# Kernel optimization log

Hardware: AMD Instinct MI355X
Metric: run time of the kernel (lower is better)

Reference implementation:

```python
import jax, jax.numpy as jnp
import numpy as np

B, N, C, H, P, K = 32, 4096, 64, 256, 8, 2


def setup_inputs() -> dict:
    key = jax.random.key(0)
    k1, k2, k3, k4 = jax.random.split(key, 4)
    s1 = 1.0 / np.sqrt(C)
    s2 = 1.0 / np.sqrt(H)
    return {
        "u_t": jax.random.normal(k1, (B, N, C), dtype=jnp.float32),
        "W1": jax.random.normal(k2, (P, C, H), dtype=jnp.float32) * s1,
        "b1": jnp.zeros((P, H), dtype=jnp.float32),
        "W2": jax.random.normal(k3, (P, H, C), dtype=jnp.float32) * s2,
        "b2": jnp.zeros((P, C), dtype=jnp.float32),
        "Wr": jax.random.normal(k4, (C, P), dtype=jnp.float32) * s1,
        "br": jnp.zeros((P,), dtype=jnp.float32),
        "top_k": K,
    }


def reference(u_t, W1, b1, W2, b2, Wr, br, top_k):
    # u_state = u_t[..., :output_channels]; here C_in == output_channels
    u_state = u_t
    # Router: mean-pool over spatial points -> per-sample logits over primitives
    pooled = jnp.mean(u_state, axis=1)                     # (B, C)
    logits = pooled @ Wr + br                              # (B, P)
    topk_vals, topk_idx = jax.lax.top_k(logits, top_k)     # (B, K)
    w = jax.nn.softmax(topk_vals, axis=-1)                 # (B, K) combine weights
    # Sparse dispatch: gather only the selected experts' params per sample
    W1e = W1[topk_idx]                                     # (B, K, C, H)
    b1e = b1[topk_idx]                                     # (B, K, H)
    W2e = W2[topk_idx]                                     # (B, K, H, C)
    b2e = b2[topk_idx]                                     # (B, K, C)
    # Primitive operator: pointwise 2-layer GELU MLP (erf gelu, torch default)
    h1 = jax.nn.gelu(jnp.einsum('bnc,bkch->bknh', u_t, W1e) + b1e[:, :, None, :],
                     approximate=False)                    # (B, K, N, H)
    delta = jnp.einsum('bknh,bkhc->bknc', h1, W2e) + b2e[:, :, None, :]  # (B, K, N, C)
    # Weighted combine: delta_sum = sum_k w_k * delta_k
    delta_sum = jnp.einsum('bknc,bk->bnc', delta, w)       # (B, N, C)
    return u_state + delta_sum
```

## Files before the change

kernel.cpp:

```cpp
#include <hip/hip_runtime.h>
#include <hip/hip_bf16.h>
#include <math.h>

#define B_ 32
#define N_ 4096
#define C_ 64
#define H_ 256
#define P_ 8
#define NPOOL 1024

typedef short bf16x8 __attribute__((ext_vector_type(8)));
typedef float f32x4 __attribute__((ext_vector_type(4)));

union BF8 { bf16x8 v; unsigned int w[4]; };

__device__ __forceinline__ unsigned short f2bf(float f) {
    union { float f; unsigned int u; } v; v.f = f;
    unsigned int r = v.u + 0x7FFFu + ((v.u >> 16) & 1u);
    return (unsigned short)(r >> 16);
}
__device__ __forceinline__ float bf2f(unsigned short h) {
    union { float f; unsigned int u; } v; v.u = ((unsigned int)h) << 16; return v.f;
}
__device__ __forceinline__ unsigned int pk_bf16(float lo, float hi) {
    unsigned int r;
    asm("v_cvt_pk_bf16_f32 %0, %1, %2" : "=v"(r) : "v"(lo), "v"(hi));
    return r;
}
__device__ __forceinline__ float gelu_w(float x, float wk) {
    float x2 = x * x;
    float y2 = x * fmaf(0.10294322f, x2, 2.30220772f);
    float e  = __builtin_amdgcn_exp2f(y2);
    float rc = __builtin_amdgcn_rcpf(e + 1.0f);
    float wx = wk * x;
    return fmaf(-wx, rc, wx);
}

__device__ __forceinline__ int hperm(int t, int d) {
    return ((t >> 1) << 5) + ((d >> 2) << 3) + ((t & 1) << 2) + (d & 3);
}

__global__ void prep_pool(const float* __restrict__ W1, const float* __restrict__ W2,
                          const float* __restrict__ b1, const float* __restrict__ u,
                          const float* __restrict__ Wr, const float* __restrict__ br,
                          unsigned short* __restrict__ W1P, unsigned short* __restrict__ W2T,
                          unsigned short* __restrict__ b1P, float* __restrict__ pooled,
                          int* __restrict__ counter, float4* __restrict__ route) {
    int bid = blockIdx.x, tid = threadIdx.x;
    if (bid < 512) {
        int oi = bid * 256 + tid;
        int e = oi >> 14, rowP = (oi >> 6) & 255, c = oi & 63;
        int h = hperm(rowP >> 4, rowP & 15);
        W1P[oi] = f2bf(W1[(e << 14) + (c << 8) + h]);
        return;
    }
    if (bid < 1024) {
        int oi = (bid - 512) * 256 + tid;
        int e = oi >> 14, c = (oi >> 8) & 63, h = oi & 255;
        W2T[oi] = f2bf(W2[(e << 14) + (h << 6) + c]);
        return;
    }
    if (bid < 1032) {
        int oi = (bid - 1024) * 256 + tid;
        int e = oi >> 8, idx = oi & 255;
        int h = hperm(idx >> 4, idx & 15);
        b1P[oi] = f2bf(b1[(e << 8) + h]);
        return;
    }
    int pb = bid - 1032;
    int b = pb >> 5, chunk = pb & 31;
    int c = tid & 63, rg = tid >> 6;
    const float* base = u + ((size_t)b * N_ + (size_t)chunk * 128) * C_;
    float s = 0.f;
    #pragma unroll 4
    for (int i = 0; i < 32; ++i) s += base[(i * 4 + rg) * C_ + c];
    __shared__ float red[4][64];
    __shared__ int isLast;
    __shared__ float lgAll[B_][P_];
    red[rg][c] = s;
    __syncthreads();
    if (tid < 64) {
        float t4 = red[0][tid] + red[1][tid] + red[2][tid] + red[3][tid];
        atomicAdd(&pooled[b * C_ + tid], t4);
        __threadfence();
    }
    __syncthreads();
    if (tid == 0) {
        int old = atomicAdd(counter, 1);
        isLast = (old == NPOOL - 1);
    }
    __syncthreads();
    if (!isLast) return;
    __threadfence();
    {
        int rb = tid >> 3, p = tid & 7;
        const float* pb2 = pooled + rb * C_;
        float sacc = br[p];
        #pragma unroll
        for (int cc = 0; cc < C_; ++cc) {
            float pv = __hip_atomic_load(&pb2[cc], __ATOMIC_RELAXED, __HIP_MEMORY_SCOPE_AGENT);
            sacc += pv * (1.0f / N_) * Wr[cc * P_ + p];
        }
        lgAll[rb][p] = sacc;
    }
    __syncthreads();
    if (tid < B_) {
        float lg[P_];
        #pragma unroll
        for (int p = 0; p < P_; ++p) lg[p] = lgAll[tid][p];
        int i0 = 0;
        #pragma unroll
        for (int p = 1; p < P_; ++p) if (lg[p] > lg[i0]) i0 = p;
        int i1 = (i0 == 0) ? 1 : 0;
        #pragma unroll
        for (int p = 0; p < P_; ++p) if (p != i0 && lg[p] > lg[i1]) i1 = p;
        float e1 = __expf(lg[i1] - lg[i0]);
        float w0 = 1.f / (1.f + e1);
        route[tid] = make_float4(w0, e1 * w0, __int_as_float(i0), __int_as_float(i1));
    }
}

__global__ __launch_bounds__(256, 2)
void moe_main(const float* __restrict__ u, const unsigned short* __restrict__ W1P,
              const unsigned short* __restrict__ W2T, const unsigned short* __restrict__ b1P,
              const float* __restrict__ b2, const float4* __restrict__ route,
              float* __restrict__ out) {
    const int tid = threadIdx.x;
    const int wv = tid >> 6, lane = tid & 63;
    const int r = lane & 15, g = lane >> 4;
    const int b = blockIdx.x >> 4;
    const int nslab = ((blockIdx.x & 15) << 2) + wv;
    const int n0 = nslab << 6;

    float4 rd = route[b];
    const float wk2[2] = { rd.x, rd.y };
    const int eidx[2] = { __float_as_int(rd.z), __float_as_int(rd.w) };

    const float* ubase = u + ((size_t)b * N_ + n0) * C_;
    bf16x8 ub[4][2];
    #pragma unroll
    for (int rt = 0; rt < 4; ++rt) {
        const float* rp = ubase + (rt * 16 + r) * C_;
        #pragma unroll
        for (int ks = 0; ks < 2; ++ks) {
            float4 lo = *(const float4*)(rp + ks * 32 + g * 8);
            float4 hi = *(const float4*)(rp + ks * 32 + g * 8 + 4);
            BF8 t;
            t.w[0] = pk_bf16(lo.x, lo.y); t.w[1] = pk_bf16(lo.z, lo.w);
            t.w[2] = pk_bf16(hi.x, hi.y); t.w[3] = pk_bf16(hi.z, hi.w);
            ub[rt][ks] = t.v;
        }
    }

    f32x4 acc2[4][4];
    #pragma unroll
    for (int ct = 0; ct < 4; ++ct)
        #pragma unroll
        for (int rt = 0; rt < 4; ++rt)
            #pragma unroll
            for (int q = 0; q < 4; ++q) acc2[ct][rt][q] = 0.f;

    for (int ke = 0; ke < 2; ++ke) {
        const int e = eidx[ke];
        const float wk = wk2[ke];
        const unsigned short* w1p = W1P + (e << 14);
        const unsigned short* w2t = W2T + (e << 14);
        const unsigned short* b1e = b1P + (e << 8);

        #pragma unroll
        for (int tp = 0; tp < 8; ++tp) {
            bf16x8 a1[2][2];
            #pragma unroll
            for (int tt = 0; tt < 2; ++tt)
                #pragma unroll
                for (int ks = 0; ks < 2; ++ks)
                    a1[tt][ks] = *(const bf16x8*)(w1p + ((tp * 32 + tt * 16 + r) << 6) + ks * 32 + g * 8);
            f32x4 acc1[2][4];
            #pragma unroll
            for (int tt = 0; tt < 2; ++tt)
                #pragma unroll
                for (int rt = 0; rt < 4; ++rt)
                    #pragma unroll
                    for (int q = 0; q < 4; ++q) acc1[tt][rt][q] = 0.f;
            #pragma unroll
            for (int ks = 0; ks < 2; ++ks)
                #pragma unroll
                for (int tt = 0; tt < 2; ++tt)
                    #pragma unroll
                    for (int rt = 0; rt < 4; ++rt)
                        acc1[tt][rt] = __builtin_amdgcn_mfma_f32_16x16x32_bf16(
                            a1[tt][ks], ub[rt][ks], acc1[tt][rt], 0, 0, 0);

            float bv[8];
            {
                const unsigned short* bp = b1e + tp * 32 + 4 * g;
                #pragma unroll
                for (int j = 0; j < 4; ++j) { bv[j] = bf2f(bp[j]); bv[4 + j] = bf2f(bp[16 + j]); }
            }
            bf16x8 a2[4];
            #pragma unroll
            for (int rt = 0; rt < 4; ++rt) {
                float gv[8];
                #pragma unroll
                for (int j = 0; j < 4; ++j) {
                    gv[j]     = gelu_w(acc1[0][rt][j] + bv[j],     wk);
                    gv[4 + j] = gelu_w(acc1[1][rt][j] + bv[4 + j], wk);
                }
                BF8 t;
                t.w[0] = pk_bf16(gv[0], gv[1]); t.w[1] = pk_bf16(gv[2], gv[3]);
                t.w[2] = pk_bf16(gv[4], gv[5]); t.w[3] = pk_bf16(gv[6], gv[7]);
                a2[rt] = t.v;
            }

            bf16x8 b2f[4];
            #pragma unroll
            for (int ct = 0; ct < 4; ++ct)
                b2f[ct] = *(const bf16x8*)(w2t + ((ct * 16 + r) << 8) + tp * 32 + g * 8);
            #pragma unroll
            for (int ct = 0; ct < 4; ++ct)
                #pragma unroll
                for (int rt = 0; rt < 4; ++rt)
                    acc2[ct][rt] = __builtin_amdgcn_mfma_f32_16x16x32_bf16(
                        a2[rt], b2f[ct], acc2[ct][rt], 0, 0, 0);
        }
    }

    float bsum[4];
    #pragma unroll
    for (int ct = 0; ct < 4; ++ct) {
        int c = ct * 16 + r;
        bsum[ct] = wk2[0] * b2[eidx[0] * C_ + c] + wk2[1] * b2[eidx[1] * C_ + c];
    }
    float* obase = out + ((size_t)b * N_ + n0) * C_;
    #pragma unroll
    for (int rt = 0; rt < 4; ++rt)
        #pragma unroll
        for (int j = 0; j < 4; ++j) {
            int row = rt * 16 + 4 * g + j;
            #pragma unroll
            for (int ct = 0; ct < 4; ++ct) {
                int c = ct * 16 + r;
                obase[row * C_ + c] = ubase[row * C_ + c] + acc2[ct][rt][j] + bsum[ct];
            }
        }
}

extern "C" void kernel_launch(void* const* d_in, const int* in_sizes, int n_in,
                              void* d_out, int out_size, void* d_ws, size_t ws_size,
                              hipStream_t stream) {
    const float* u  = (const float*)d_in[0];
    const float* W1 = (const float*)d_in[1];
    const float* b1 = (const float*)d_in[2];
    const float* W2 = (const float*)d_in[3];
    const float* b2 = (const float*)d_in[4];
    const float* Wr = (const float*)d_in[5];
    const float* br = (const float*)d_in[6];
    float* out = (float*)d_out;

    char* ws = (char*)d_ws;
    float* pooled        = (float*)ws;
    int* counter         = (int*)(ws + 8192);
    float4* route        = (float4*)(ws + 8256);
    unsigned short* b1P  = (unsigned short*)(ws + 8768);
    unsigned short* W1P  = (unsigned short*)(ws + 16384);
    unsigned short* W2T  = (unsigned short*)(ws + 16384 + 262144);

    hipMemsetAsync(ws, 0, 8256, stream);
    prep_pool<<<2056, 256, 0, stream>>>(W1, W2, b1, u, Wr, br, W1P, W2T, b1P, pooled, counter, route);
    moe_main<<<512, 256, 0, stream>>>(u, W1P, W2T, b1P, b2, route, out);
}
```

Measured before the change: 167.3 us.

## Double-buffer expert weight loads and transpose weights through LDS in prep

The main MoE kernel now software-pipelines its per-tile weight and bias fetches with two register buffers, so the next tile's loads are in flight while the current tile's MFMAs and GELU run. The second GEMM is also interleaved per row tile instead of after all GELUs. The prep kernel packs W1/W2 to bf16 with 16 blocks that transpose through shared memory using coalesced float4 reads, replacing 1032 blocks of strided scalar gathers. The cost is higher register pressure from the double buffers, which could reduce occupancy, and far fewer prep blocks doing the conversion.

Measured after the change: 171.3 us. 1.02x slower.

```diff
diff --git a/kernel.cpp b/kernel.cpp
--- a/kernel.cpp
+++ b/kernel.cpp
@@ -35,8 +35,8 @@
     float wx = wk * x;
     return fmaf(-wx, rc, wx);
 }
-
-__device__ __forceinline__ int hperm(int t, int d) {
+__device__ __forceinline__ int hperm_p(int p) {
+    int t = p >> 4, d = p & 15;
     return ((t >> 1) << 5) + ((d >> 2) << 3) + ((t & 1) << 2) + (d & 3);
 }
 
@@ -46,41 +46,77 @@
                           unsigned short* __restrict__ W1P, unsigned short* __restrict__ W2T,
                           unsigned short* __restrict__ b1P, float* __restrict__ pooled,
                           int* __restrict__ counter, float4* __restrict__ route) {
-    int bid = blockIdx.x, tid = threadIdx.x;
-    if (bid < 512) {
-        int oi = bid * 256 + tid;
-        int e = oi >> 14, rowP = (oi >> 6) & 255, c = oi & 63;
-        int h = hperm(rowP >> 4, rowP & 15);
-        W1P[oi] = f2bf(W1[(e << 14) + (c << 8) + h]);
+    __shared__ union {
+        unsigned short t[256 * 66];
+        unsigned short s[64 * 258];
+        struct { float red[4][64]; float lgAll[B_][P_]; } pr;
+    } sh;
+    __shared__ int isLast;
+
+    const int bid = blockIdx.x, tid = threadIdx.x;
+
+    if (bid < 16) {
+        const int e = bid >> 1, m = bid & 1;
+        if (m == 0) {
+            const float* src = W1 + (e << 14);
+            #pragma unroll
+            for (int i = 0; i < 16; ++i) {
+                int c = i * 4 + (tid >> 6), h4 = (tid & 63) * 4;
+                float4 v = *(const float4*)(src + c * 256 + h4);
+                sh.t[(h4 + 0) * 66 + c] = f2bf(v.x);
+                sh.t[(h4 + 1) * 66 + c] = f2bf(v.y);
+                sh.t[(h4 + 2) * 66 + c] = f2bf(v.z);
+                sh.t[(h4 + 3) * 66 + c] = f2bf(v.w);
+            }
+            __syncthreads();
+            unsigned short* dst = W1P + (e << 14);
+            #pragma unroll
+            for (int i = 0; i < 32; ++i) {
+                int p = i * 8 + (tid >> 5), c2 = (tid & 31) * 2;
+                int h = hperm_p(p);
+                *(ushort2*)(dst + (p << 6) + c2) = *(const ushort2*)&sh.t[h * 66 + c2];
+            }
+        } else {
+            const float* src = W2 + (e << 14);
+            #pragma unroll
+            for (int i = 0; i < 16; ++i) {
+                int h = i * 16 + (tid >> 4), c4 = (tid & 15) * 4;
+                float4 v = *(const float4*)(src + (h << 6) + c4);
+                sh.s[(c4 + 0) * 258 + h] = f2bf(v.x);
+                sh.s[(c4 + 1) * 258 + h] = f2bf(v.y);
+                sh.s[(c4 + 2) * 258 + h] = f2bf(v.z);
+                sh.s[(c4 + 3) * 258 + h] = f2bf(v.w);
+            }
+            __syncthreads();
+            unsigned short* dst = W2T + (e << 14);
+            #pragma unroll
+            for (int i = 0; i < 32; ++i) {
+                int c = i * 2 + (tid >> 7), h2 = (tid & 127) * 2;
+                *(ushort2*)(dst + (c << 8) + h2) = *(const ushort2*)&sh.s[c * 258 + h2];
+            }
+        }
         return;
     }
-    if (bid < 1024) {
-        int oi = (bid - 512) * 256 + tid;
-        int e = oi >> 14, c = (oi >> 8) & 63, h = oi & 255;
-        W2T[oi] = f2bf(W2[(e << 14) + (h << 6) + c]);
+    if (bid == 16) {
+        #pragma unroll
+        for (int i = 0; i < 8; ++i) {
+            int oi = i * 256 + tid;
+            int e = oi >> 8, p = oi & 255;
+            b1P[oi] = f2bf(b1[(e << 8) + hperm_p(p)]);
+        }
         return;
     }
-    if (bid < 1032) {
-        int oi = (bid - 1024) * 256 + tid;
-        int e = oi >> 8, idx = oi & 255;
-        int h = hperm(idx >> 4, idx & 15);
-        b1P[oi] = f2bf(b1[(e << 8) + h]);
-        return;
-    }
-    int pb = bid - 1032;
+    int pb = bid - 17;
     int b = pb >> 5, chunk = pb & 31;
     int c = tid & 63, rg = tid >> 6;
     const float* base = u + ((size_t)b * N_ + (size_t)chunk * 128) * C_;
     float s = 0.f;
     #pragma unroll 4
     for (int i = 0; i < 32; ++i) s += base[(i * 4 + rg) * C_ + c];
-    __shared__ float red[4][64];
-    __shared__ int isLast;
-    __shared__ float lgAll[B_][P_];
-    red[rg][c] = s;
+    sh.pr.red[rg][c] = s;
     __syncthreads();
     if (tid < 64) {
-        float t4 = red[0][tid] + red[1][tid] + red[2][tid] + red[3][tid];
+        float t4 = sh.pr.red[0][tid] + sh.pr.red[1][tid] + sh.pr.red[2][tid] + sh.pr.red[3][tid];
         atomicAdd(&pooled[b * C_ + tid], t4);
         __threadfence();
     }
@@ -101,13 +137,13 @@
             float pv = __hip_atomic_load(&pb2[cc], __ATOMIC_RELAXED, __HIP_MEMORY_SCOPE_AGENT);
             sacc += pv * (1.0f / N_) * Wr[cc * P_ + p];
         }
-        lgAll[rb][p] = sacc;
+        sh.pr.lgAll[rb][p] = sacc;
     }
     __syncthreads();
     if (tid < B_) {
         float lg[P_];
         #pragma unroll
-        for (int p = 0; p < P_; ++p) lg[p] = lgAll[tid][p];
+        for (int p = 0; p < P_; ++p) lg[p] = sh.pr.lgAll[tid][p];
         int i0 = 0;
         #pragma unroll
         for (int p = 1; p < P_; ++p) if (lg[p] > lg[i0]) i0 = p;
@@ -119,6 +155,56 @@
         route[tid] = make_float4(w0, e1 * w0, __int_as_float(i0), __int_as_float(i1));
     }
 }
+
+__device__ __forceinline__ void comp_tp(const bf16x8 (&A)[2][2], const bf16x8 (&Bw)[4],
+                                        ushort4 bva, ushort4 bvb, float wk,
+                                        const bf16x8 (&ub)[4][2], f32x4 (&acc2)[4][4]) {
+    f32x4 c1[2][4];
+    #pragma unroll
+    for (int tt = 0; tt < 2; ++tt)
+        #pragma unroll
+        for (int rt = 0; rt < 4; ++rt)
+            #pragma unroll
+            for (int q = 0; q < 4; ++q) c1[tt][rt][q] = 0.f;
+    #pragma unroll
+    for (int ks = 0; ks < 2; ++ks)
+        #pragma unroll
+        for (int tt = 0; tt < 2; ++tt)
+            #pragma unroll
+            for (int rt = 0; rt < 4; ++rt)
+                c1[tt][rt] = __builtin_amdgcn_mfma_f32_16x16x32_bf16(A[tt][ks], ub[rt][ks], c1[tt][rt], 0, 0, 0);
+    float bv[8];
+    bv[0] = bf2f(bva.x); bv[1] = bf2f(bva.y); bv[2] = bf2f(bva.z); bv[3] = bf2f(bva.w);
+    bv[4] = bf2f(bvb.x); bv[5] = bf2f(bvb.y); bv[6] = bf2f(bvb.z); bv[7] = bf2f(bvb.w);
+    #pragma unroll
+    for (int rt = 0; rt < 4; ++rt) {
+        float gv[8];
+        #pragma unroll
+        for (int j = 0; j < 4; ++j) {
+            gv[j]     = gelu_w(c1[0][rt][j] + bv[j],     wk);
+            gv[4 + j] = gelu_w(c1[1][rt][j] + bv[4 + j], wk);
+        }
+        BF8 t;
+        t.w[0] = pk_bf16(gv[0], gv[1]); t.w[1] = pk_bf16(gv[2], gv[3]);
+        t.w[2] = pk_bf16(gv[4], gv[5]); t.w[3] = pk_bf16(gv[6], gv[7]);
+        bf16x8 a2 = t.v;
+        #pragma unroll
+        for (int ct = 0; ct < 4; ++ct)
+            acc2[ct][rt] = __builtin_amdgcn_mfma_f32_16x16x32_bf16(a2, Bw[ct], acc2[ct][rt], 0, 0, 0);
+    }
+}
+
+#define LOADS(A, Bw, bva, bvb, tp) \
+    A[0][0] = *(const bf16x8*)(w1p + (((tp) * 32 +  0 + r) << 6) +  0 + g * 8); \
+    A[0][1] = *(const bf16x8*)(w1p + (((tp) * 32 +  0 + r) << 6) + 32 + g * 8); \
+    A[1][0] = *(const bf16x8*)(w1p + (((tp) * 32 + 16 + r) << 6) +  0 + g * 8); \
+    A[1][1] = *(const bf16x8*)(w1p + (((tp) * 32 + 16 + r) << 6) + 32 + g * 8); \
+    Bw[0] = *(const bf16x8*)(w2t + (( 0 + r) << 8) + (tp) * 32 + g * 8); \
+    Bw[1] = *(const bf16x8*)(w2t + ((16 + r) << 8) + (tp) * 32 + g * 8); \
+    Bw[2] = *(const bf16x8*)(w2t + ((32 + r) << 8) + (tp) * 32 + g * 8); \
+    Bw[3] = *(const bf16x8*)(w2t + ((48 + r) << 8) + (tp) * 32 + g * 8); \
+    bva = *(const ushort4*)(b1e + (tp) * 32 + 4 * g); \
+    bvb = *(const ushort4*)(b1e + (tp) * 32 + 16 + 4 * g);
 
 __global__ __launch_bounds__(256, 2)
 void moe_main(const float* __restrict__ u, const unsigned short* __restrict__ W1P,
@@ -133,8 +219,6 @@
     const int n0 = nslab << 6;
 
     float4 rd = route[b];
-    const float wk2[2] = { rd.x, rd.y };
-    const int eidx[2] = { __float_as_int(rd.z), __float_as_int(rd.w) };
 
     const float* ubase = u + ((size_t)b * N_ + n0) * C_;
     bf16x8 ub[4][2];
@@ -160,76 +244,32 @@
             #pragma unroll
             for (int q = 0; q < 4; ++q) acc2[ct][rt][q] = 0.f;
 
+    #pragma unroll
     for (int ke = 0; ke < 2; ++ke) {
-        const int e = eidx[ke];
-        const float wk = wk2[ke];
+        const int e = ke ? __float_as_int(rd.w) : __float_as_int(rd.z);
+        const float wk = ke ? rd.y : rd.x;
         const unsigned short* w1p = W1P + (e << 14);
         const unsigned short* w2t = W2T + (e << 14);
         const unsigned short* b1e = b1P + (e << 8);
 
-        #pragma unroll
-        for (int tp = 0; tp < 8; ++tp) {
-            bf16x8 a1[2][2];
-            #pragma unroll
-            for (int tt = 0; tt < 2; ++tt)
-                #pragma unroll
-                for (int ks = 0; ks < 2; ++ks)
-                    a1[tt][ks] = *(const bf16x8*)(w1p + ((tp * 32 + tt * 16 + r) << 6) + ks * 32 + g * 8);
-            f32x4 acc1[2][4];
-            #pragma unroll
-            for (int tt = 0; tt < 2; ++tt)
-                #pragma unroll
-                for (int rt = 0; rt < 4; ++rt)
-                    #pragma unroll
-                    for (int q = 0; q < 4; ++q) acc1[tt][rt][q] = 0.f;
-            #pragma unroll
-            for (int ks = 0; ks < 2; ++ks)
-                #pragma unroll
-                for (int tt = 0; tt < 2; ++tt)
-                    #pragma unroll
-                    for (int rt = 0; rt < 4; ++rt)
-                        acc1[tt][rt] = __builtin_amdgcn_mfma_f32_16x16x32_bf16(
-                            a1[tt][ks], ub[rt][ks], acc1[tt][rt], 0, 0, 0);
-
-            float bv[8];
-            {
-                const unsigned short* bp = b1e + tp * 32 + 4 * g;
-                #pragma unroll
-                for (int j = 0; j < 4; ++j) { bv[j] = bf2f(bp[j]); bv[4 + j] = bf2f(bp[16 + j]); }
-            }
-            bf16x8 a2[4];
-            #pragma unroll
-            for (int rt = 0; rt < 4; ++rt) {
-                float gv[8];
-                #pragma unroll
-                for (int j = 0; j < 4; ++j) {
-                    gv[j]     = gelu_w(acc1[0][rt][j] + bv[j],     wk);
-                    gv[4 + j] = gelu_w(acc1[1][rt][j] + bv[4 + j], wk);
-                }
-                BF8 t;
-                t.w[0] = pk_bf16(gv[0], gv[1]); t.w[1] = pk_bf16(gv[2], gv[3]);
-                t.w[2] = pk_bf16(gv[4], gv[5]); t.w[3] = pk_bf16(gv[6], gv[7]);
-                a2[rt] = t.v;
-            }
-
-            bf16x8 b2f[4];
-            #pragma unroll
-            for (int ct = 0; ct < 4; ++ct)
-                b2f[ct] = *(const bf16x8*)(w2t + ((ct * 16 + r) << 8) + tp * 32 + g * 8);
-            #pragma unroll
-            for (int ct = 0; ct < 4; ++ct)
-                #pragma unroll
-                for (int rt = 0; rt < 4; ++rt)
-                    acc2[ct][rt] = __builtin_amdgcn_mfma_f32_16x16x32_bf16(
-                        a2[rt], b2f[ct], acc2[ct][rt], 0, 0, 0);
-        }
-    }
-
+        bf16x8 Aa[2][2], Ba[4]; ushort4 va0, va1;
+        bf16x8 Ab[2][2], Bb[4]; ushort4 vb0, vb1;
+        LOADS(Aa, Ba, va0, va1, 0)
+        #pragma unroll
+        for (int tpp = 0; tpp < 4; ++tpp) {
+            LOADS(Ab, Bb, vb0, vb1, 2 * tpp + 1)
+            comp_tp(Aa, Ba, va0, va1, wk, ub, acc2);
+            if (tpp < 3) { LOADS(Aa, Ba, va0, va1, 2 * tpp + 2) }
+            comp_tp(Ab, Bb, vb0, vb1, wk, ub, acc2);
+        }
+    }
+
+    const int e0 = __float_as_int(rd.z), e1i = __float_as_int(rd.w);
     float bsum[4];
     #pragma unroll
     for (int ct = 0; ct < 4; ++ct) {
         int c = ct * 16 + r;
-        bsum[ct] = wk2[0] * b2[eidx[0] * C_ + c] + wk2[1] * b2[eidx[1] * C_ + c];
+        bsum[ct] = rd.x * b2[e0 * C_ + c] + rd.y * b2[e1i * C_ + c];
     }
     float* obase = out + ((size_t)b * N_ + n0) * C_;
     #pragma unroll
@@ -266,6 +306,6 @@
     unsigned short* W2T  = (unsigned short*)(ws + 16384 + 262144);
 
     hipMemsetAsync(ws, 0, 8256, stream);
-    prep_pool<<<2056, 256, 0, stream>>>(W1, W2, b1, u, Wr, br, W1P, W2T, b1P, pooled, counter, route);
+    prep_pool<<<1041, 256, 0, stream>>>(W1, W2, b1, u, Wr, br, W1P, W2T, b1P, pooled, counter, route);
     moe_main<<<512, 256, 0, stream>>>(u, W1P, W2T, b1P, b2, route, out);
 }
```
